# Optimization experiments

Measured on AMD Instinct MI355X. Metric: run time of the kernel, lower is better.

## Reference

```python
import jax, jax.numpy as jnp
import numpy as np

N = 200_000      # n_reflns
NIMG = 500       # n_images
DMETA = 24       # metadata features
WIDTH = 32       # mlp_width
HID = 64         # hidden_units = 2*width (FeedForward default)
DEPTH = 20       # mlp_depth
NPOST = 2        # Normal posterior: (loc, scale)
EPS = 1e-12
KLW = 0.01       # scaling_kl_weight


def setup_inputs() -> dict:
    key = jax.random.key(0)
    ks = jax.random.split(key, 10)
    metadata = jax.random.normal(ks[0], (N, DMETA), jnp.float32)
    iobs = jax.random.normal(ks[1], (N, 1), jnp.float32)
    sigiobs = jax.random.uniform(ks[2], (N, 1), jnp.float32)
    image_ids = jnp.sort(jax.random.randint(ks[3], (N,), 0, NIMG)).astype(jnp.int32)
    n_reflns_per_image = jnp.bincount(image_ids, length=NIMG).astype(jnp.int32)
    d_img = DMETA + 2  # concat(metadata, iobs, sigiobs)
    w_img_in = jax.random.normal(ks[4], (d_img, WIDTH), jnp.float32) / np.float32(np.sqrt(d_img))
    b_img_in = jnp.zeros((WIDTH,), jnp.float32)
    w_scale_in = jax.random.normal(ks[5], (DMETA, WIDTH), jnp.float32) / np.float32(np.sqrt(DMETA))
    b_scale_in = jnp.zeros((WIDTH,), jnp.float32)
    # shared residual FeedForward stack (share_weights=True): x + W2 @ relu(W1 @ x)
    mlp_w1 = jax.random.normal(ks[6], (DEPTH, WIDTH, HID), jnp.float32) / np.float32(np.sqrt(WIDTH))
    mlp_b1 = jnp.zeros((DEPTH, HID), jnp.float32)
    mlp_w2 = jax.random.normal(ks[7], (DEPTH, HID, WIDTH), jnp.float32) * np.float32(0.1 / np.sqrt(HID))
    mlp_b2 = jnp.zeros((DEPTH, WIDTH), jnp.float32)
    w_out = jax.random.normal(ks[8], (WIDTH, NPOST), jnp.float32) / np.float32(np.sqrt(WIDTH))
    b_out = jnp.zeros((NPOST,), jnp.float32)
    return {
        'metadata': metadata, 'iobs': iobs, 'sigiobs': sigiobs,
        'w_img_in': w_img_in, 'b_img_in': b_img_in,
        'w_scale_in': w_scale_in, 'b_scale_in': b_scale_in,
        'mlp_w1': mlp_w1, 'mlp_b1': mlp_b1, 'mlp_w2': mlp_w2, 'mlp_b2': mlp_b2,
        'w_out': w_out, 'b_out': b_out,
        'image_ids_in_this_batch': image_ids,
        'n_reflns_per_image': n_reflns_per_image,
        'mc_samples': 32,
    }


def _mlp(h, w1, b1, w2, b2):
    # depth residual FF blocks, weights stacked along leading DEPTH axis
    def block(h, ws):
        wa, ba, wb, bb = ws
        h = h + (jax.nn.relu(h @ wa + ba) @ wb + bb)
        return h, None
    h, _ = jax.lax.scan(block, h, (w1, b1, w2, b2))
    return h


def reference(metadata, iobs, sigiobs,
              w_img_in, b_img_in, w_scale_in, b_scale_in,
              mlp_w1, mlp_b1, mlp_w2, mlp_b2, w_out, b_out,
              image_ids_in_this_batch, n_reflns_per_image, mc_samples):
    image = jnp.concatenate([metadata, iobs, sigiobs], axis=-1)   # (N, DMETA+2)
    h = image @ w_img_in + b_img_in                               # (N, W)
    h = _mlp(h, mlp_w1, mlp_b1, mlp_w2, mlp_b2)
    nimg = n_reflns_per_image.shape[0]
    sums = jax.ops.segment_sum(h, image_ids_in_this_batch, num_segments=nimg)
    counts = jnp.maximum(n_reflns_per_image, 1).astype(h.dtype)[:, None]
    pooled = sums / counts                                        # (NIMG, W) image-average pool
    s = metadata @ w_scale_in + b_scale_in + pooled[image_ids_in_this_batch]
    s = _mlp(s, mlp_w1, mlp_b1, mlp_w2, mlp_b2)                   # shared weights
    params = s @ w_out + b_out                                    # (N, 2)
    loc = params[:, 0]
    scale = jax.nn.softplus(params[:, 1]) + EPS
    # rsample from Normal(loc, scale), mc_samples draws
    noise = jax.random.normal(jax.random.key(42), (mc_samples, loc.shape[0]), loc.dtype)
    z = loc + scale * noise                                       # (S, N)
    # MC KL estimate: mean_s[log q(z) - log p(z)], p = Laplace(0, 1)
    log_q = -0.5 * jnp.square(noise) - jnp.log(scale) - np.float32(0.5 * np.log(2.0 * np.pi))
    log_p = -jnp.abs(z) - np.float32(np.log(2.0))
    kl_div = KLW * jnp.mean(log_q - log_p, axis=0)                # (N,)
    return z.T, kl_div
```

## Files before the change

### kernel.cpp

```cpp
#include <hip/hip_runtime.h>
#include <stdint.h>

#define N_ROWS 200000
#define NIMG   500
#define DMETA  24
#define WIDTH  32
#define HID    64
#define DEPTH  20
#define MC     32

#define LSTRIDE_F 68
#define TILE_F    (16 * LSTRIDE_F)

#define WB    64000
#define LSTR  17920
#define OFF_WIH (WB + DEPTH * LSTR)
#define OFF_WIL (OFF_WIH + 2048)
#define OFF_WSH (OFF_WIH + 4096)
#define OFF_WSL (OFF_WIH + 6144)

typedef __attribute__((ext_vector_type(8))) short bf16x8;
typedef __attribute__((ext_vector_type(4))) float f32x4;

#define MFMA(a, b, acc) __builtin_amdgcn_mfma_f32_16x16x32_bf16((a), (b), (acc), 0, 0, 0)

__device__ __forceinline__ uint32_t rotl32(uint32_t x, int r) {
    return (x << r) | (x >> (32 - r));
}

__device__ __forceinline__ uint32_t tf_bits(uint32_t j) {
    const uint32_t ks1 = 42u, ks2 = 0x1BD11BDAu ^ 42u;
    uint32_t x0 = 0u, x1 = j + ks1;
#define R4(a,b,c,d) \
    x0 += x1; x1 = rotl32(x1,(a)); x1 ^= x0; \
    x0 += x1; x1 = rotl32(x1,(b)); x1 ^= x0; \
    x0 += x1; x1 = rotl32(x1,(c)); x1 ^= x0; \
    x0 += x1; x1 = rotl32(x1,(d)); x1 ^= x0;
    R4(13,15,26,6)  x0 += ks1; x1 += ks2 + 1u;
    R4(17,29,16,24) x0 += ks2; x1 += 0u + 2u;
    R4(13,15,26,6)                x1 += ks1 + 3u;
    R4(17,29,16,24) x0 += ks1; x1 += ks2 + 4u;
    R4(13,15,26,6)  x0 += ks2; x1 += 0u + 5u;
#undef R4
    return x0 ^ x1;
}

__device__ __forceinline__ float bits_to_normal(uint32_t b) {
    float f = __uint_as_float((b >> 9) | 0x3f800000u) - 1.0f;
    const float lo = -0.99999994f;
    float u = fmaxf(lo, f * 2.0f + lo);
    return 1.41421356f * erfinvf(u);
}

__device__ __forceinline__ void split1(float x, short& hi, short& lo) {
    uint32_t b = __float_as_uint(x);
    uint32_t a = b + 0x8000u;
    hi = (short)(a >> 16);
    float r = x - __uint_as_float(a & 0xFFFF0000u);
    lo = (short)(__float_as_uint(r) >> 16);
}

__device__ __forceinline__ void split8p(const float* x, bf16x8& hi, bf16x8& lo) {
    uint32_t hu[4], lu[4];
#pragma unroll
    for (int p = 0; p < 4; ++p) {
        float x0 = x[2 * p], x1 = x[2 * p + 1];
        uint32_t h;
        asm("v_cvt_pk_bf16_f32 %0, %1, %2" : "=v"(h) : "v"(x0), "v"(x1));
        float r0 = x0 - __uint_as_float(h << 16);
        float r1 = x1 - __uint_as_float(h & 0xFFFF0000u);
        uint32_t l;
        asm("v_cvt_pk_bf16_f32 %0, %1, %2" : "=v"(l) : "v"(r0), "v"(r1));
        hu[p] = h;
        lu[p] = l;
    }
    __builtin_memcpy(&hi, hu, 16);
    __builtin_memcpy(&lo, lu, 16);
}

__device__ __forceinline__ void cvt8p(const float* x, bf16x8& hi) {
    uint32_t hu[4];
#pragma unroll
    for (int p = 0; p < 4; ++p) {
        uint32_t h;
        asm("v_cvt_pk_bf16_f32 %0, %1, %2" : "=v"(h) : "v"(x[2 * p]), "v"(x[2 * p + 1]));
        hu[p] = h;
    }
    __builtin_memcpy(&hi, hu, 16);
}

__device__ __forceinline__ void mlp20_x2(
    float* hC0, float* hC1, float* smw, const char* __restrict__ wsb,
    int lane, int q, int c) {
    const int ldsR = c * LSTRIDE_F + q * 8;
    const int ldsW = q * 4 * LSTRIDE_F + c;
    uint32_t offA  = (uint32_t)(WB + (lane << 4));
    uint32_t offB  = offA + 4096u;
    uint32_t offC  = offA + 8192u;
    uint32_t offD  = offA + 12288u;
    uint32_t offB1 = (uint32_t)(WB + 16384 + (c << 4));
    uint32_t offB2 = (uint32_t)(WB + 17408 + (c << 4));
#pragma unroll 1
    for (int l = 0; l < DEPTH; ++l) {
        float a0[8], a1[8];
#pragma unroll
        for (int t = 0; t < 2; ++t)
#pragma unroll
            for (int r = 0; r < 4; ++r)
                smw[ldsW + r * LSTRIDE_F + t * 16] = hC0[t * 4 + r];
        {
            f32x4 v0 = *(const f32x4*)(smw + ldsR);
            f32x4 v1 = *(const f32x4*)(smw + ldsR + 4);
#pragma unroll
            for (int j = 0; j < 4; ++j) { a0[j] = v0[j]; a0[4 + j] = v1[j]; }
        }
#pragma unroll
        for (int t = 0; t < 2; ++t)
#pragma unroll
            for (int r = 0; r < 4; ++r)
                smw[ldsW + r * LSTRIDE_F + t * 16] = hC1[t * 4 + r];
        {
            f32x4 u0 = *(const f32x4*)(smw + ldsR);
            f32x4 u1 = *(const f32x4*)(smw + ldsR + 4);
#pragma unroll
            for (int j = 0; j < 4; ++j) { a1[j] = u0[j]; a1[4 + j] = u1[j]; }
        }
        bf16x8 ah0, ah1;
        cvt8p(a0, ah0);
        cvt8p(a1, ah1);
        float C1v0[16], C1v1[16];
#pragma unroll
        for (int t = 0; t < 4; ++t) {
            uint32_t o = (t < 2 ? offA : offB) + (uint32_t)((t & 1) << 11);
            bf16x8 bh = *(const bf16x8*)(wsb + o);
            bf16x8 bl = *(const bf16x8*)(wsb + o + 1024);
            f32x4 b1q = *(const f32x4*)(wsb + offB1 + (uint32_t)(t << 8));
            f32x4 acc = MFMA(ah0, bh, b1q);
            acc = MFMA(ah0, bl, acc);
            f32x4 acd = MFMA(ah1, bh, b1q);
            acd = MFMA(ah1, bl, acd);
#pragma unroll
            for (int r = 0; r < 4; ++r) {
                C1v0[t * 4 + r] = fmaxf(acc[r], 0.0f);
                C1v1[t * 4 + r] = fmaxf(acd[r], 0.0f);
            }
        }
        bf16x8 xh0[2], xh1[2];
#pragma unroll
        for (int t = 0; t < 4; ++t)
#pragma unroll
            for (int r = 0; r < 4; ++r)
                smw[ldsW + r * LSTRIDE_F + t * 16] = C1v0[t * 4 + r];
#pragma unroll
        for (int kf = 0; kf < 2; ++kf) {
            f32x4 ea = *(const f32x4*)(smw + ldsR + kf * 32);
            f32x4 eb = *(const f32x4*)(smw + ldsR + kf * 32 + 4);
            float e[8];
#pragma unroll
            for (int j = 0; j < 4; ++j) { e[j] = ea[j]; e[4 + j] = eb[j]; }
            cvt8p(e, xh0[kf]);
        }
#pragma unroll
        for (int t = 0; t < 4; ++t)
#pragma unroll
            for (int r = 0; r < 4; ++r)
                smw[ldsW + r * LSTRIDE_F + t * 16] = C1v1[t * 4 + r];
#pragma unroll
        for (int kf = 0; kf < 2; ++kf) {
            f32x4 ea = *(const f32x4*)(smw + ldsR + kf * 32);
            f32x4 eb = *(const f32x4*)(smw + ldsR + kf * 32 + 4);
            float e[8];
#pragma unroll
            for (int j = 0; j < 4; ++j) { e[j] = ea[j]; e[4 + j] = eb[j]; }
            cvt8p(e, xh1[kf]);
        }
        f32x4 b2q0 = *(const f32x4*)(wsb + offB2);
        f32x4 b2q1 = *(const f32x4*)(wsb + offB2 + 256u);
        f32x4 acc0[2], acc1[2];
#pragma unroll
        for (int r = 0; r < 4; ++r) {
            acc0[0][r] = hC0[r] + b2q0[r];
            acc0[1][r] = hC0[4 + r] + b2q1[r];
            acc1[0][r] = hC1[r] + b2q0[r];
            acc1[1][r] = hC1[4 + r] + b2q1[r];
        }
#pragma unroll
        for (int kf = 0; kf < 2; ++kf) {
#pragma unroll
            for (int t2 = 0; t2 < 2; ++t2) {
                uint32_t o = (kf ? offD : offC) + (uint32_t)(t2 << 11);
                bf16x8 bh = *(const bf16x8*)(wsb + o);
                bf16x8 bl = *(const bf16x8*)(wsb + o + 1024);
                acc0[t2] = MFMA(xh0[kf], bh, acc0[t2]);
                acc0[t2] = MFMA(xh0[kf], bl, acc0[t2]);
                acc1[t2] = MFMA(xh1[kf], bh, acc1[t2]);
                acc1[t2] = MFMA(xh1[kf], bl, acc1[t2]);
            }
        }
#pragma unroll
        for (int t2 = 0; t2 < 2; ++t2)
#pragma unroll
            for (int r = 0; r < 4; ++r) {
                hC0[t2 * 4 + r] = acc0[t2][r];
                hC1[t2 * 4 + r] = acc1[t2][r];
            }
        offA += LSTR; offB += LSTR; offC += LSTR; offD += LSTR;
        offB1 += LSTR; offB2 += LSTR;
    }
}

__device__ __forceinline__ void input_proj(
    const bf16x8& ah, const bf16x8& al, const short* __restrict__ wfh,
    const short* __restrict__ wfl, const float* __restrict__ bias,
    float* hC, int lane, int c) {
#pragma unroll
    for (int t = 0; t < 2; ++t) {
        bf16x8 bh = *(const bf16x8*)(wfh + ((t << 9) + (lane << 3)));
        bf16x8 bl = *(const bf16x8*)(wfl + ((t << 9) + (lane << 3)));
        float bb = bias[16 * t + c];
        f32x4 acc = {bb, bb, bb, bb};
        acc = MFMA(ah, bh, acc); acc = MFMA(ah, bl, acc); acc = MFMA(al, bh, acc);
#pragma unroll
        for (int r = 0; r < 4; ++r) hC[t * 4 + r] = acc[r];
    }
}

__global__ __launch_bounds__(256) void prep_kernel(
    const float* __restrict__ w1, const float* __restrict__ w2,
    const float* __restrict__ wimg, const float* __restrict__ wsc,
    const float* __restrict__ b1, const float* __restrict__ b2,
    char* __restrict__ wsb) {
    int t = blockIdx.x * 256 + threadIdx.x;
    float* sums = (float*)wsb;
    if (t < 16000) { sums[t] = 0.0f; return; }
    t -= 16000;
    if (t < 40960) {
        int l = t >> 11, r = t & 2047, tt = r >> 9, r2 = r & 511;
        int lane = r2 >> 3, j = r2 & 7;
        int k = (lane >> 4) * 8 + j, n = 16 * tt + (lane & 15);
        short h, lo;
        split1(w1[l * 2048 + k * 64 + n], h, lo);
        char* base = wsb + WB + l * LSTR + tt * 2048 + 2 * r2;
        *(short*)(base) = h;
        *(short*)(base + 1024) = lo;
        return;
    }
    t -= 40960;
    if (t < 40960) {
        int l = t >> 11, r = t & 2047, kf = r >> 10, r2 = r & 1023;
        int t2 = r2 >> 9, r3 = r2 & 511, lane = r3 >> 3, j = r3 & 7;
        int k = kf * 32 + (lane >> 4) * 8 + j, n = 16 * t2 + (lane & 15);
        short h, lo;
        split1(w2[l * 2048 + k * 32 + n], h, lo);
        char* base = wsb + WB + l * LSTR + 8192 + (kf * 2 + t2) * 2048 + 2 * r3;
        *(short*)(base) = h;
        *(short*)(base + 1024) = lo;
        return;
    }
    t -= 40960;
    if (t < 1024) {
        int tt = t >> 9, r = t & 511, lane = r >> 3, j = r & 7;
        int k = (lane >> 4) * 8 + j, n = 16 * tt + (lane & 15);
        float v = (k < 26) ? wimg[k * 32 + n] : 0.0f;
        short h, lo;
        split1(v, h, lo);
        ((short*)(wsb + OFF_WIH))[t] = h;
        ((short*)(wsb + OFF_WIL))[t] = lo;
        return;
    }
    t -= 1024;
    if (t < 1024) {
        int tt = t >> 9, r = t & 511, lane = r >> 3, j = r & 7;
        int k = (lane >> 4) * 8 + j, n = 16 * tt + (lane & 15);
        float v = (k < 24) ? wsc[k * 32 + n] : 0.0f;
        short h, lo;
        split1(v, h, lo);
        ((short*)(wsb + OFF_WSH))[t] = h;
        ((short*)(wsb + OFF_WSL))[t] = lo;
        return;
    }
    t -= 1024;
    if (t < 5120) {
        int l = t >> 8, r = t & 255;
        int tt = r >> 6, cc = (r >> 2) & 15;
        *(float*)(wsb + WB + l * LSTR + 16384 + 4 * r) = b1[l * 64 + tt * 16 + cc];
        return;
    }
    t -= 5120;
    if (t < 2560) {
        int l = t >> 7, r = t & 127;
        int t2 = r >> 6, cc = (r >> 2) & 15;
        *(float*)(wsb + WB + l * LSTR + 17408 + 4 * r) = b2[l * 32 + t2 * 16 + cc];
        return;
    }
}

__device__ __forceinline__ void load_xfrag(
    const float* __restrict__ md, const float* __restrict__ iobs,
    const float* __restrict__ sig, int base, int q, int c,
    bf16x8& ah, bf16x8& al) {
    float xa[8];
    if (q < 3) {
        const f32x4* rp = (const f32x4*)(md + (size_t)(base + c) * DMETA + q * 8);
        f32x4 v0 = rp[0], v1 = rp[1];
#pragma unroll
        for (int j = 0; j < 4; ++j) { xa[j] = v0[j]; xa[4 + j] = v1[j]; }
    } else {
        xa[0] = iobs ? iobs[base + c] : 0.0f;
        xa[1] = sig ? sig[base + c] : 0.0f;
#pragma unroll
        for (int j = 2; j < 8; ++j) xa[j] = 0.0f;
    }
    split8p(xa, ah, al);
}

__global__ __launch_bounds__(128, 4) void pass_a(
    const float* __restrict__ md, const float* __restrict__ iobs,
    const float* __restrict__ sig, const float* __restrict__ bimg,
    const char* __restrict__ wsb, const int* __restrict__ ids,
    float* __restrict__ sums) {
    __shared__ __attribute__((aligned(16))) float smat[2][TILE_F];
    int lane = threadIdx.x & 63, w = threadIdx.x >> 6;
    int q = lane >> 4, c = lane & 15;
    int i0 = (blockIdx.x * 2 + w) * 32;
    float* smw = &smat[w][0];

    bf16x8 ah0, al0, ah1, al1;
    load_xfrag(md, iobs, sig, i0, q, c, ah0, al0);
    load_xfrag(md, iobs, sig, i0 + 16, q, c, ah1, al1);

    float hC0[8], hC1[8];
    input_proj(ah0, al0, (const short*)(wsb + OFF_WIH), (const short*)(wsb + OFF_WIL),
               bimg, hC0, lane, c);
    input_proj(ah1, al1, (const short*)(wsb + OFF_WIH), (const short*)(wsb + OFF_WIL),
               bimg, hC1, lane, c);

    mlp20_x2(hC0, hC1, smw, wsb, lane, q, c);

#pragma unroll
    for (int tile = 0; tile < 2; ++tile) {
        const float* hC = tile ? hC1 : hC0;
        int tb = i0 + tile * 16;
        bool uni = (ids[tb] == ids[tb + 15]);
        if (uni) {
            int id = ids[tb];
#pragma unroll
            for (int t = 0; t < 2; ++t) {
                float s = (hC[t * 4 + 0] + hC[t * 4 + 1]) + (hC[t * 4 + 2] + hC[t * 4 + 3]);
                s += __shfl_xor(s, 16, 64);
                s += __shfl_xor(s, 32, 64);
                if (q == 0) atomicAdd(&sums[id * 32 + 16 * t + c], s);
            }
        } else {
            int idv[4];
#pragma unroll
            for (int r = 0; r < 4; ++r) idv[r] = ids[tb + q * 4 + r];
#pragma unroll
            for (int t = 0; t < 2; ++t)
#pragma unroll
                for (int r = 0; r < 4; ++r)
                    atomicAdd(&sums[idv[r] * 32 + 16 * t + c], hC[t * 4 + r]);
        }
    }
}

__global__ __launch_bounds__(256) void normalize_kernel(float* __restrict__ sums,
                                                        const int* __restrict__ cnts) {
    int t = blockIdx.x * 256 + threadIdx.x;
    if (t < NIMG * WIDTH) {
        int img = t >> 5;
        float cc = (float)max(cnts[img], 1);
        sums[t] = sums[t] / cc;
    }
}

__global__ __launch_bounds__(128, 4) void pass_b(
    const float* __restrict__ md, const float* __restrict__ bsc,
    const char* __restrict__ wsb, const float* __restrict__ wout,
    const float* __restrict__ bout, const int* __restrict__ ids,
    const float* __restrict__ pooled, float* __restrict__ out) {
    __shared__ __attribute__((aligned(16))) float smat[2][TILE_F];
    __shared__ float sls[2][64];
    int lane = threadIdx.x & 63, w = threadIdx.x >> 6;
    int q = lane >> 4, c = lane & 15;
    int i0 = (blockIdx.x * 2 + w) * 32;
    float* smw = &smat[w][0];

    bf16x8 ah0, al0, ah1, al1;
    load_xfrag(md, nullptr, nullptr, i0, q, c, ah0, al0);
    load_xfrag(md, nullptr, nullptr, i0 + 16, q, c, ah1, al1);

    float hC0[8], hC1[8];
    input_proj(ah0, al0, (const short*)(wsb + OFF_WSH), (const short*)(wsb + OFF_WSL),
               bsc, hC0, lane, c);
    input_proj(ah1, al1, (const short*)(wsb + OFF_WSH), (const short*)(wsb + OFF_WSL),
               bsc, hC1, lane, c);
#pragma unroll
    for (int tile = 0; tile < 2; ++tile) {
        float* hC = tile ? hC1 : hC0;
        int tb = i0 + tile * 16;
        int idv[4];
#pragma unroll
        for (int r = 0; r < 4; ++r) idv[r] = ids[tb + q * 4 + r];
#pragma unroll
        for (int t = 0; t < 2; ++t)
#pragma unroll
            for (int r = 0; r < 4; ++r)
                hC[t * 4 + r] += pooled[idv[r] * 32 + 16 * t + c];
    }

    mlp20_x2(hC0, hC1, smw, wsb, lane, q, c);

    float wo0[2], wo1[2];
#pragma unroll
    for (int t = 0; t < 2; ++t) {
        float2 wv = ((const float2*)wout)[16 * t + c];
        wo0[t] = wv.x; wo1[t] = wv.y;
    }
#pragma unroll
    for (int tile = 0; tile < 2; ++tile) {
        const float* hC = tile ? hC1 : hC0;
        float p0r[4], p1r[4];
#pragma unroll
        for (int r = 0; r < 4; ++r) {
            p0r[r] = hC[r] * wo0[0] + hC[4 + r] * wo0[1];
            p1r[r] = hC[r] * wo1[0] + hC[4 + r] * wo1[1];
        }
#pragma unroll
        for (int m = 1; m < 16; m <<= 1) {
#pragma unroll
            for (int r = 0; r < 4; ++r) {
                p0r[r] += __shfl_xor(p0r[r], m, 64);
                p1r[r] += __shfl_xor(p1r[r], m, 64);
            }
        }
        if (c == 0) {
#pragma unroll
            for (int r = 0; r < 4; ++r) {
                float loc = p0r[r] + bout[0];
                float pb = p1r[r] + bout[1];
                float scale = fmaxf(pb, 0.0f) + log1pf(expf(-fabsf(pb))) + 1e-12f;
                sls[w][tile * 16 + q * 4 + r] = loc;
                sls[w][32 + tile * 16 + q * 4 + r] = scale;
            }
        }
    }

    int ro = lane & 31, half = lane >> 5;
    int row = i0 + ro;
    float L = sls[w][ro];
    float S = sls[w][32 + ro];
    float lsg = logf(S);
    float kp = 0.0f;
    float* zrow = out + (size_t)row * MC + half * 16;
#pragma unroll 4
    for (int s4 = 0; s4 < 4; ++s4) {
        f32x4 zv;
#pragma unroll
        for (int jj = 0; jj < 4; ++jj) {
            int t = half * 16 + s4 * 4 + jj;
            uint32_t j = (uint32_t)(t * N_ROWS) + (uint32_t)row;
            float n = bits_to_normal(tf_bits(j));
            float z = fmaf(S, n, L);
            zv[jj] = z;
            kp += fmaf(-0.5f, n * n, fabsf(z));
        }
        *(f32x4*)(zrow + s4 * 4) = zv;
    }
    kp += __shfl_xor(kp, 32, 64);
    if (half == 0) {
        out[(size_t)N_ROWS * MC + row] =
            0.01f * (kp * (1.0f / 32.0f) - lsg - 0.91893853320467274f + 0.69314718055994531f);
    }
}

extern "C" void kernel_launch(void* const* d_in, const int* in_sizes, int n_in,
                              void* d_out, int out_size, void* d_ws, size_t ws_size,
                              hipStream_t stream) {
    const float* md   = (const float*)d_in[0];
    const float* iobs = (const float*)d_in[1];
    const float* sig  = (const float*)d_in[2];
    const float* wimg = (const float*)d_in[3];
    const float* bimg = (const float*)d_in[4];
    const float* wsc  = (const float*)d_in[5];
    const float* bsc  = (const float*)d_in[6];
    const float* w1   = (const float*)d_in[7];
    const float* b1   = (const float*)d_in[8];
    const float* w2   = (const float*)d_in[9];
    const float* b2   = (const float*)d_in[10];
    const float* wout = (const float*)d_in[11];
    const float* bout = (const float*)d_in[12];
    const int* ids    = (const int*)d_in[13];
    const int* cnts   = (const int*)d_in[14];
    float* out = (float*)d_out;
    char* wsb = (char*)d_ws;
    float* sums = (float*)wsb;

    const int nblk = N_ROWS / 64;
    prep_kernel<<<421, 256, 0, stream>>>(w1, w2, wimg, wsc, b1, b2, wsb);
    pass_a<<<nblk, 128, 0, stream>>>(md, iobs, sig, bimg, wsb, ids, sums);
    normalize_kernel<<<(NIMG * WIDTH + 255) / 256, 256, 0, stream>>>(sums, cnts);
    pass_b<<<nblk, 128, 0, stream>>>(md, bsc, wsb, wout, bout, ids, sums, out);
}
```

Baseline: 321.4 us.

## Process four 16-row tiles per wave in the MLP to reuse weight loads

```diff
diff --git a/kernel.cpp b/kernel.cpp
--- a/kernel.cpp
+++ b/kernel.cpp
@@ -89,9 +89,61 @@
     __builtin_memcpy(&hi, hu, 16);
 }
 
-__device__ __forceinline__ void mlp20_x2(
-    float* hC0, float* hC1, float* smw, const char* __restrict__ wsb,
-    int lane, int q, int c) {
+__device__ __forceinline__ void rt1(const float* hC, float* smw, int ldsW,
+                                    int ldsR, float* a) {
+#pragma unroll
+    for (int t = 0; t < 2; ++t)
+#pragma unroll
+        for (int r = 0; r < 4; ++r)
+            smw[ldsW + r * LSTRIDE_F + t * 16] = hC[t * 4 + r];
+    f32x4 v0 = *(const f32x4*)(smw + ldsR);
+    f32x4 v1 = *(const f32x4*)(smw + ldsR + 4);
+#pragma unroll
+    for (int j = 0; j < 4; ++j) { a[j] = v0[j]; a[4 + j] = v1[j]; }
+}
+
+__device__ __forceinline__ void rt2(const float* C1, float* smw, int ldsW,
+                                    int ldsR, bf16x8* xh) {
+#pragma unroll
+    for (int t = 0; t < 4; ++t)
+#pragma unroll
+        for (int r = 0; r < 4; ++r)
+            smw[ldsW + r * LSTRIDE_F + t * 16] = C1[t * 4 + r];
+#pragma unroll
+    for (int kf = 0; kf < 2; ++kf) {
+        f32x4 ea = *(const f32x4*)(smw + ldsR + kf * 32);
+        f32x4 eb = *(const f32x4*)(smw + ldsR + kf * 32 + 4);
+        float e[8];
+#pragma unroll
+        for (int j = 0; j < 4; ++j) { e[j] = ea[j]; e[4 + j] = eb[j]; }
+        cvt8p(e, xh[kf]);
+    }
+}
+
+__device__ __forceinline__ void stage1_pair(
+    const bf16x8& ahA, const bf16x8& ahB, const char* __restrict__ wsb,
+    uint32_t offA, uint32_t offB, uint32_t offB1, float* C1A, float* C1B) {
+#pragma unroll
+    for (int t = 0; t < 4; ++t) {
+        uint32_t o = (t < 2 ? offA : offB) + (uint32_t)((t & 1) << 11);
+        bf16x8 bh = *(const bf16x8*)(wsb + o);
+        bf16x8 bl = *(const bf16x8*)(wsb + o + 1024);
+        f32x4 b1q = *(const f32x4*)(wsb + offB1 + (uint32_t)(t << 8));
+        f32x4 acc = MFMA(ahA, bh, b1q);
+        acc = MFMA(ahA, bl, acc);
+        f32x4 acd = MFMA(ahB, bh, b1q);
+        acd = MFMA(ahB, bl, acd);
+#pragma unroll
+        for (int r = 0; r < 4; ++r) {
+            C1A[t * 4 + r] = fmaxf(acc[r], 0.0f);
+            C1B[t * 4 + r] = fmaxf(acd[r], 0.0f);
+        }
+    }
+}
+
+__device__ __forceinline__ void mlp20_x4(
+    float* hC0, float* hC1, float* hC2, float* hC3,
+    float* smw, const char* __restrict__ wsb, int lane, int q, int c) {
     const int ldsR = c * LSTRIDE_F + q * 8;
     const int ldsW = q * 4 * LSTRIDE_F + c;
     uint32_t offA  = (uint32_t)(WB + (lane << 4));
@@ -103,86 +155,35 @@
 #pragma unroll 1
     for (int l = 0; l < DEPTH; ++l) {
         float a0[8], a1[8];
-#pragma unroll
-        for (int t = 0; t < 2; ++t)
-#pragma unroll
-            for (int r = 0; r < 4; ++r)
-                smw[ldsW + r * LSTRIDE_F + t * 16] = hC0[t * 4 + r];
-        {
-            f32x4 v0 = *(const f32x4*)(smw + ldsR);
-            f32x4 v1 = *(const f32x4*)(smw + ldsR + 4);
-#pragma unroll
-            for (int j = 0; j < 4; ++j) { a0[j] = v0[j]; a0[4 + j] = v1[j]; }
-        }
-#pragma unroll
-        for (int t = 0; t < 2; ++t)
-#pragma unroll
-            for (int r = 0; r < 4; ++r)
-                smw[ldsW + r * LSTRIDE_F + t * 16] = hC1[t * 4 + r];
-        {
-            f32x4 u0 = *(const f32x4*)(smw + ldsR);
-            f32x4 u1 = *(const f32x4*)(smw + ldsR + 4);
-#pragma unroll
-            for (int j = 0; j < 4; ++j) { a1[j] = u0[j]; a1[4 + j] = u1[j]; }
-        }
+        rt1(hC0, smw, ldsW, ldsR, a0);
+        rt1(hC1, smw, ldsW, ldsR, a1);
         bf16x8 ah0, ah1;
         cvt8p(a0, ah0);
         cvt8p(a1, ah1);
         float C1v0[16], C1v1[16];
-#pragma unroll
-        for (int t = 0; t < 4; ++t) {
-            uint32_t o = (t < 2 ? offA : offB) + (uint32_t)((t & 1) << 11);
-            bf16x8 bh = *(const bf16x8*)(wsb + o);
-            bf16x8 bl = *(const bf16x8*)(wsb + o + 1024);
-            f32x4 b1q = *(const f32x4*)(wsb + offB1 + (uint32_t)(t << 8));
-            f32x4 acc = MFMA(ah0, bh, b1q);
-            acc = MFMA(ah0, bl, acc);
-            f32x4 acd = MFMA(ah1, bh, b1q);
-            acd = MFMA(ah1, bl, acd);
-#pragma unroll
-            for (int r = 0; r < 4; ++r) {
-                C1v0[t * 4 + r] = fmaxf(acc[r], 0.0f);
-                C1v1[t * 4 + r] = fmaxf(acd[r], 0.0f);
-            }
-        }
-        bf16x8 xh0[2], xh1[2];
-#pragma unroll
-        for (int t = 0; t < 4; ++t)
-#pragma unroll
-            for (int r = 0; r < 4; ++r)
-                smw[ldsW + r * LSTRIDE_F + t * 16] = C1v0[t * 4 + r];
-#pragma unroll
-        for (int kf = 0; kf < 2; ++kf) {
-            f32x4 ea = *(const f32x4*)(smw + ldsR + kf * 32);
-            f32x4 eb = *(const f32x4*)(smw + ldsR + kf * 32 + 4);
-            float e[8];
-#pragma unroll
-            for (int j = 0; j < 4; ++j) { e[j] = ea[j]; e[4 + j] = eb[j]; }
-            cvt8p(e, xh0[kf]);
-        }
-#pragma unroll
-        for (int t = 0; t < 4; ++t)
-#pragma unroll
-            for (int r = 0; r < 4; ++r)
-                smw[ldsW + r * LSTRIDE_F + t * 16] = C1v1[t * 4 + r];
-#pragma unroll
-        for (int kf = 0; kf < 2; ++kf) {
-            f32x4 ea = *(const f32x4*)(smw + ldsR + kf * 32);
-            f32x4 eb = *(const f32x4*)(smw + ldsR + kf * 32 + 4);
-            float e[8];
-#pragma unroll
-            for (int j = 0; j < 4; ++j) { e[j] = ea[j]; e[4 + j] = eb[j]; }
-            cvt8p(e, xh1[kf]);
-        }
+        stage1_pair(ah0, ah1, wsb, offA, offB, offB1, C1v0, C1v1);
+        float a2[8], a3[8];
+        rt1(hC2, smw, ldsW, ldsR, a2);
+        rt1(hC3, smw, ldsW, ldsR, a3);
+        bf16x8 ah2, ah3;
+        cvt8p(a2, ah2);
+        cvt8p(a3, ah3);
+        float C1v2[16], C1v3[16];
+        stage1_pair(ah2, ah3, wsb, offA, offB, offB1, C1v2, C1v3);
+        bf16x8 xh0[2], xh1[2], xh2[2], xh3[2];
+        rt2(C1v0, smw, ldsW, ldsR, xh0);
+        rt2(C1v1, smw, ldsW, ldsR, xh1);
+        rt2(C1v2, smw, ldsW, ldsR, xh2);
+        rt2(C1v3, smw, ldsW, ldsR, xh3);
         f32x4 b2q0 = *(const f32x4*)(wsb + offB2);
         f32x4 b2q1 = *(const f32x4*)(wsb + offB2 + 256u);
-        f32x4 acc0[2], acc1[2];
+        f32x4 A0[2], A1[2], A2[2], A3[2];
 #pragma unroll
         for (int r = 0; r < 4; ++r) {
-            acc0[0][r] = hC0[r] + b2q0[r];
-            acc0[1][r] = hC0[4 + r] + b2q1[r];
-            acc1[0][r] = hC1[r] + b2q0[r];
-            acc1[1][r] = hC1[4 + r] + b2q1[r];
+            A0[0][r] = hC0[r] + b2q0[r];  A0[1][r] = hC0[4 + r] + b2q1[r];
+            A1[0][r] = hC1[r] + b2q0[r];  A1[1][r] = hC1[4 + r] + b2q1[r];
+            A2[0][r] = hC2[r] + b2q0[r];  A2[1][r] = hC2[4 + r] + b2q1[r];
+            A3[0][r] = hC3[r] + b2q0[r];  A3[1][r] = hC3[4 + r] + b2q1[r];
         }
 #pragma unroll
         for (int kf = 0; kf < 2; ++kf) {
@@ -191,18 +192,24 @@
                 uint32_t o = (kf ? offD : offC) + (uint32_t)(t2 << 11);
                 bf16x8 bh = *(const bf16x8*)(wsb + o);
                 bf16x8 bl = *(const bf16x8*)(wsb + o + 1024);
-                acc0[t2] = MFMA(xh0[kf], bh, acc0[t2]);
-                acc0[t2] = MFMA(xh0[kf], bl, acc0[t2]);
-                acc1[t2] = MFMA(xh1[kf], bh, acc1[t2]);
-                acc1[t2] = MFMA(xh1[kf], bl, acc1[t2]);
+                A0[t2] = MFMA(xh0[kf], bh, A0[t2]);
+                A0[t2] = MFMA(xh0[kf], bl, A0[t2]);
+                A1[t2] = MFMA(xh1[kf], bh, A1[t2]);
+                A1[t2] = MFMA(xh1[kf], bl, A1[t2]);
+                A2[t2] = MFMA(xh2[kf], bh, A2[t2]);
+                A2[t2] = MFMA(xh2[kf], bl, A2[t2]);
+                A3[t2] = MFMA(xh3[kf], bh, A3[t2]);
+                A3[t2] = MFMA(xh3[kf], bl, A3[t2]);
             }
         }
 #pragma unroll
         for (int t2 = 0; t2 < 2; ++t2)
 #pragma unroll
             for (int r = 0; r < 4; ++r) {
-                hC0[t2 * 4 + r] = acc0[t2][r];
-                hC1[t2 * 4 + r] = acc1[t2][r];
+                hC0[t2 * 4 + r] = A0[t2][r];
+                hC1[t2 * 4 + r] = A1[t2][r];
+                hC2[t2 * 4 + r] = A2[t2][r];
+                hC3[t2 * 4 + r] = A3[t2][r];
             }
         offA += LSTR; offB += LSTR; offC += LSTR; offD += LSTR;
         offB1 += LSTR; offB2 += LSTR;
@@ -314,7 +321,7 @@
     split8p(xa, ah, al);
 }
 
-__global__ __launch_bounds__(128, 4) void pass_a(
+__global__ __launch_bounds__(128, 3) void pass_a(
     const float* __restrict__ md, const float* __restrict__ iobs,
     const float* __restrict__ sig, const float* __restrict__ bimg,
     const char* __restrict__ wsb, const int* __restrict__ ids,
@@ -322,25 +329,32 @@
     __shared__ __attribute__((aligned(16))) float smat[2][TILE_F];
     int lane = threadIdx.x & 63, w = threadIdx.x >> 6;
     int q = lane >> 4, c = lane & 15;
-    int i0 = (blockIdx.x * 2 + w) * 32;
+    int gw = blockIdx.x * 2 + w;
+    if (gw > 3124) return;
+    int R = gw * 64;
     float* smw = &smat[w][0];
 
-    bf16x8 ah0, al0, ah1, al1;
-    load_xfrag(md, iobs, sig, i0, q, c, ah0, al0);
-    load_xfrag(md, iobs, sig, i0 + 16, q, c, ah1, al1);
-
-    float hC0[8], hC1[8];
-    input_proj(ah0, al0, (const short*)(wsb + OFF_WIH), (const short*)(wsb + OFF_WIL),
-               bimg, hC0, lane, c);
-    input_proj(ah1, al1, (const short*)(wsb + OFF_WIH), (const short*)(wsb + OFF_WIL),
-               bimg, hC1, lane, c);
-
-    mlp20_x2(hC0, hC1, smw, wsb, lane, q, c);
-
-#pragma unroll
-    for (int tile = 0; tile < 2; ++tile) {
-        const float* hC = tile ? hC1 : hC0;
-        int tb = i0 + tile * 16;
+    float hC0[8], hC1[8], hC2[8], hC3[8];
+    {
+        bf16x8 ah, al;
+        const short* wfh = (const short*)(wsb + OFF_WIH);
+        const short* wfl = (const short*)(wsb + OFF_WIL);
+        load_xfrag(md, iobs, sig, R, q, c, ah, al);
+        input_proj(ah, al, wfh, wfl, bimg, hC0, lane, c);
+        load_xfrag(md, iobs, sig, R + 16, q, c, ah, al);
+        input_proj(ah, al, wfh, wfl, bimg, hC1, lane, c);
+        load_xfrag(md, iobs, sig, R + 32, q, c, ah, al);
+        input_proj(ah, al, wfh, wfl, bimg, hC2, lane, c);
+        load_xfrag(md, iobs, sig, R + 48, q, c, ah, al);
+        input_proj(ah, al, wfh, wfl, bimg, hC3, lane, c);
+    }
+
+    mlp20_x4(hC0, hC1, hC2, hC3, smw, wsb, lane, q, c);
+
+#pragma unroll
+    for (int tile = 0; tile < 4; ++tile) {
+        const float* hC = tile == 0 ? hC0 : tile == 1 ? hC1 : tile == 2 ? hC2 : hC3;
+        int tb = R + tile * 16;
         bool uni = (ids[tb] == ids[tb + 15]);
         if (uni) {
             int id = ids[tb];
@@ -374,31 +388,38 @@
     }
 }
 
-__global__ __launch_bounds__(128, 4) void pass_b(
+__global__ __launch_bounds__(128, 3) void pass_b(
     const float* __restrict__ md, const float* __restrict__ bsc,
     const char* __restrict__ wsb, const float* __restrict__ wout,
     const float* __restrict__ bout, const int* __restrict__ ids,
     const float* __restrict__ pooled, float* __restrict__ out) {
     __shared__ __attribute__((aligned(16))) float smat[2][TILE_F];
-    __shared__ float sls[2][64];
+    __shared__ float sls[2][128];
     int lane = threadIdx.x & 63, w = threadIdx.x >> 6;
     int q = lane >> 4, c = lane & 15;
-    int i0 = (blockIdx.x * 2 + w) * 32;
+    int gw = blockIdx.x * 2 + w;
+    if (gw > 3124) return;
+    int R = gw * 64;
     float* smw = &smat[w][0];
 
-    bf16x8 ah0, al0, ah1, al1;
-    load_xfrag(md, nullptr, nullptr, i0, q, c, ah0, al0);
-    load_xfrag(md, nullptr, nullptr, i0 + 16, q, c, ah1, al1);
-
-    float hC0[8], hC1[8];
-    input_proj(ah0, al0, (const short*)(wsb + OFF_WSH), (const short*)(wsb + OFF_WSL),
-               bsc, hC0, lane, c);
-    input_proj(ah1, al1, (const short*)(wsb + OFF_WSH), (const short*)(wsb + OFF_WSL),
-               bsc, hC1, lane, c);
-#pragma unroll
-    for (int tile = 0; tile < 2; ++tile) {
-        float* hC = tile ? hC1 : hC0;
-        int tb = i0 + tile * 16;
+    float hC0[8], hC1[8], hC2[8], hC3[8];
+    {
+        bf16x8 ah, al;
+        const short* wfh = (const short*)(wsb + OFF_WSH);
+        const short* wfl = (const short*)(wsb + OFF_WSL);
+        load_xfrag(md, nullptr, nullptr, R, q, c, ah, al);
+        input_proj(ah, al, wfh, wfl, bsc, hC0, lane, c);
+        load_xfrag(md, nullptr, nullptr, R + 16, q, c, ah, al);
+        input_proj(ah, al, wfh, wfl, bsc, hC1, lane, c);
+        load_xfrag(md, nullptr, nullptr, R + 32, q, c, ah, al);
+        input_proj(ah, al, wfh, wfl, bsc, hC2, lane, c);
+        load_xfrag(md, nullptr, nullptr, R + 48, q, c, ah, al);
+        input_proj(ah, al, wfh, wfl, bsc, hC3, lane, c);
+    }
+#pragma unroll
+    for (int tile = 0; tile < 4; ++tile) {
+        float* hC = tile == 0 ? hC0 : tile == 1 ? hC1 : tile == 2 ? hC2 : hC3;
+        int tb = R + tile * 16;
         int idv[4];
 #pragma unroll
         for (int r = 0; r < 4; ++r) idv[r] = ids[tb + q * 4 + r];
@@ -409,7 +430,7 @@
                 hC[t * 4 + r] += pooled[idv[r] * 32 + 16 * t + c];
     }
 
-    mlp20_x2(hC0, hC1, smw, wsb, lane, q, c);
+    mlp20_x4(hC0, hC1, hC2, hC3, smw, wsb, lane, q, c);
 
     float wo0[2], wo1[2];
 #pragma unroll
@@ -418,8 +439,8 @@
         wo0[t] = wv.x; wo1[t] = wv.y;
     }
 #pragma unroll
-    for (int tile = 0; tile < 2; ++tile) {
-        const float* hC = tile ? hC1 : hC0;
+    for (int tile = 0; tile < 4; ++tile) {
+        const float* hC = tile == 0 ? hC0 : tile == 1 ? hC1 : tile == 2 ? hC2 : hC3;
         float p0r[4], p1r[4];
 #pragma unroll
         for (int r = 0; r < 4; ++r) {
@@ -441,24 +462,23 @@
                 float pb = p1r[r] + bout[1];
                 float scale = fmaxf(pb, 0.0f) + log1pf(expf(-fabsf(pb))) + 1e-12f;
                 sls[w][tile * 16 + q * 4 + r] = loc;
-                sls[w][32 + tile * 16 + q * 4 + r] = scale;
+                sls[w][64 + tile * 16 + q * 4 + r] = scale;
             }
         }
     }
 
-    int ro = lane & 31, half = lane >> 5;
-    int row = i0 + ro;
-    float L = sls[w][ro];
-    float S = sls[w][32 + ro];
+    int row = R + lane;
+    float L = sls[w][lane];
+    float S = sls[w][64 + lane];
     float lsg = logf(S);
     float kp = 0.0f;
-    float* zrow = out + (size_t)row * MC + half * 16;
-#pragma unroll 4
-    for (int s4 = 0; s4 < 4; ++s4) {
+    float* zrow = out + (size_t)row * MC;
+#pragma unroll 8
+    for (int s4 = 0; s4 < 8; ++s4) {
         f32x4 zv;
 #pragma unroll
         for (int jj = 0; jj < 4; ++jj) {
-            int t = half * 16 + s4 * 4 + jj;
+            int t = s4 * 4 + jj;
             uint32_t j = (uint32_t)(t * N_ROWS) + (uint32_t)row;
             float n = bits_to_normal(tf_bits(j));
             float z = fmaf(S, n, L);
@@ -467,11 +487,8 @@
         }
         *(f32x4*)(zrow + s4 * 4) = zv;
     }
-    kp += __shfl_xor(kp, 32, 64);
-    if (half == 0) {
-        out[(size_t)N_ROWS * MC + row] =
-            0.01f * (kp * (1.0f / 32.0f) - lsg - 0.91893853320467274f + 0.69314718055994531f);
-    }
+    out[(size_t)N_ROWS * MC + row] =
+        0.01f * (kp * (1.0f / 32.0f) - lsg - 0.91893853320467274f + 0.69314718055994531f);
 }
 
 extern "C" void kernel_launch(void* const* d_in, const int* in_sizes, int n_in,
@@ -496,7 +513,7 @@
     char* wsb = (char*)d_ws;
     float* sums = (float*)wsb;
 
-    const int nblk = N_ROWS / 64;
+    const int nblk = 1563;
     prep_kernel<<<421, 256, 0, stream>>>(w1, w2, wimg, wsc, b1, b2, wsb);
     pass_a<<<nblk, 128, 0, stream>>>(md, iobs, sig, bimg, wsb, ids, sums);
     normalize_kernel<<<(NIMG * WIDTH + 255) / 256, 256, 0, stream>>>(sums, cnts);
```

Measured after the change: 341.8 us. 1.06x slower.
